# Performance work log

Measured on AMD Instinct MI355X. Metric: run time of the kernel, lower is better.

## Reference

```python
import jax, jax.numpy as jnp
import numpy as np


def conv1d(x, w, b, pad):
    # x: [B,C,T], w: [O,I,K]
    y = jax.lax.conv_general_dilated(x, w, (1,), [(pad, pad)],
                                     dimension_numbers=('NCH', 'OIH', 'NCH'))
    return y + b[None, :, None]


def setup_inputs() -> dict:
    key = jax.random.key(0)
    ks = jax.random.split(key, 16)
    s = 0.05
    return {
        'x':    jax.random.normal(ks[0], (1024, 512), dtype=jnp.float32),
        'w1':   jax.random.normal(ks[1], (5, 1, 3), dtype=jnp.float32) * s,
        'b1':   jnp.zeros((5,), jnp.float32),
        'w2':   jax.random.normal(ks[2], (10, 5, 5), dtype=jnp.float32) * s,
        'b2':   jnp.zeros((10,), jnp.float32),
        'w3':   jax.random.normal(ks[3], (10, 10, 7), dtype=jnp.float32) * s,
        'b3':   jnp.zeros((10,), jnp.float32),
        'code': jax.random.uniform(ks[4], (10, 32), dtype=jnp.float32),
        'd1w':  jax.random.normal(ks[5], (10, 10, 5), dtype=jnp.float32) * s,
        'd1b':  jnp.zeros((10,), jnp.float32),
        'd2w':  jax.random.normal(ks[6], (10, 10, 5), dtype=jnp.float32) * s,
        'd2b':  jnp.zeros((10,), jnp.float32),
        'fcw':  jax.random.normal(ks[7], (512, 5120), dtype=jnp.float32) * 0.01,
        'fcb':  jnp.zeros((512,), jnp.float32),
    }


def reference(x, w1, b1, w2, b2, w3, b3, code, d1w, d1b, d2w, d2b, fcw, fcb):
    B = x.shape[0]
    h = x[:, None, :]                                   # [B,1,512]
    h = jax.nn.relu(conv1d(h, w1, b1, 1))               # [B,5,512]
    h = jax.nn.relu(conv1d(h, w2, b2, 2))               # [B,10,512]
    h = jnp.tanh(conv1d(h, w3, b3, 3))                  # [B,10,512]
    # squared distance: sum_c (h[b,c,t] - code[c,k])^2 -> [B,512,32]
    x2 = jnp.sum(h * h, axis=1)                         # [B,512]
    cross = jnp.einsum('bct,ck->btk', h, code)          # [B,512,32]
    c2 = jnp.sum(code * code, axis=0)                   # [32]
    dist = x2[:, :, None] - 2.0 * cross + c2[None, None, :]
    prob = jax.nn.softmax(-dist, axis=-1)               # [B,512,32]
    q = jnp.einsum('btk,ck->btc', prob, code)           # [B,512,10]
    h = q.transpose(0, 2, 1)                            # [B,10,512]
    h = jax.nn.relu(conv1d(h, d1w, d1b, 2))
    h = jax.nn.relu(conv1d(h, d2w, d2b, 2))
    flat = h.reshape(B, -1)                             # [B,5120]
    return jnp.tanh(flat @ fcw.T + fcb)                 # [B,512]
```

## Files before the change

### kernel.cpp

```cpp
#include <hip/hip_runtime.h>
#include <hip/hip_bf16.h>

#define TT 512
#define XS 520
#define XH 4
#define RS 16
#define RH 8
#define NROW 528
#define K_FC 5120

typedef _Float16 hh2 __attribute__((ext_vector_type(2)));
typedef _Float16 h8 __attribute__((ext_vector_type(8)));
typedef float f32x16 __attribute__((ext_vector_type(16)));
typedef __attribute__((address_space(1))) const void GAS;
typedef __attribute__((address_space(3))) void LAS;

__device__ __forceinline__ float fast_tanh(float v) {
    float e = __expf(2.0f * v);
    return 1.0f - 2.0f / (e + 1.0f);
}
__device__ __forceinline__ unsigned pk(float a, float b) {
    return __builtin_bit_cast(unsigned, __builtin_amdgcn_cvt_pkrtz(a, b));
}

__global__ __launch_bounds__(256) void prep_kernel(
    const float* __restrict__ fcw, _Float16* __restrict__ fcw_h,
    const float* __restrict__ w2, const float* __restrict__ w3,
    const float* __restrict__ d1w, const float* __restrict__ d2w,
    const float* __restrict__ code, uint4* __restrict__ wtab,
    unsigned* __restrict__ c2tab)
{
    if (blockIdx.x < 1280) {
        int i = blockIdx.x * 256 + threadIdx.x;
        float4 a = ((const float4*)fcw)[i * 2];
        float4 b = ((const float4*)fcw)[i * 2 + 1];
        h8 v;
        v[0] = (_Float16)a.x; v[1] = (_Float16)a.y; v[2] = (_Float16)a.z; v[3] = (_Float16)a.w;
        v[4] = (_Float16)b.x; v[5] = (_Float16)b.y; v[6] = (_Float16)b.z; v[7] = (_Float16)b.w;
        *(h8*)&fcw_h[(size_t)i * 8] = v;
        return;
    }
    const int i = (blockIdx.x - 1280) * 256 + threadIdx.x;
    if (i < 1600) {
        const int lane = i & 63;
        const int o = lane & 31;
        const int hi = lane >> 5;
        h8 v = {};
        if (i < 320) {
            const int j = i >> 6;
            #pragma unroll
            for (int e = 0; e < 8; ++e) {
                int k = hi * 8 + e;
                if (o < 10 && k < 5) v[e] = (_Float16)w2[(o * 5 + k) * 5 + j];
            }
        } else if (i < 768) {
            const int j = (i - 320) >> 6;
            #pragma unroll
            for (int e = 0; e < 8; ++e) {
                int k = hi * 8 + e;
                if (o < 10 && k < 10) v[e] = (_Float16)w3[(o * 10 + k) * 7 + j];
            }
        } else if (i < 1088) {
            const int j = (i - 768) >> 6;
            #pragma unroll
            for (int e = 0; e < 8; ++e) {
                int k = hi * 8 + e;
                if (o < 10 && k < 10) v[e] = (_Float16)d1w[(o * 10 + k) * 5 + j];
            }
        } else if (i < 1408) {
            const int j = (i - 1088) >> 6;
            #pragma unroll
            for (int e = 0; e < 8; ++e) {
                int k = hi * 8 + e;
                if (o < 10 && k < 10) v[e] = (_Float16)d2w[(o * 10 + k) * 5 + j];
            }
        } else if (i < 1472) {
            #pragma unroll
            for (int e = 0; e < 8; ++e) {
                int ch = hi * 8 + e;
                if (ch < 10) v[e] = (_Float16)(2.0f * code[ch * 32 + o]);
            }
        } else {
            const int ks = (i - 1472) >> 6;
            #pragma unroll
            for (int e = 0; e < 8; ++e) {
                int kc = ks * 16 + hi * 8 + e;
                if (o < 10) v[e] = (_Float16)code[o * 32 + kc];
            }
        }
        wtab[i] = __builtin_bit_cast(uint4, v);
    } else if (i < 1632) {
        int k = i - 1600;
        float s = 0.f;
        for (int c = 0; c < 10; ++c) { float cv = code[c * 32 + k]; s = fmaf(cv, cv, s); }
        c2tab[k] = __float_as_uint(4.0f - s);
    }
}

template<int J, int P, int ACT>
__device__ __forceinline__ void conv_stage(
    const _Float16* __restrict__ src, _Float16* __restrict__ dst,
    const uint4* __restrict__ wtab, int wbase, const float* __restrict__ sb)
{
    const int tid = threadIdx.x;
    const int lane = tid & 63;
    const int wv = tid >> 6;
    const int l31 = lane & 31;
    const int hi = lane >> 5;

    uint4 wf[J];
    #pragma unroll
    for (int j = 0; j < J; ++j) wf[j] = wtab[wbase + j * 64 + lane];
    float bias[6];
    #pragma unroll
    for (int r = 0; r < 6; ++r) bias[r] = sb[(r & 3) + 8 * (r >> 2) + 4 * hi];

    #pragma unroll
    for (int tile = 0; tile < 4; ++tile) {
        const int tcol = wv * 128 + tile * 32 + l31;
        f32x16 acc = {};
        #pragma unroll
        for (int j = 0; j < J; ++j) {
            h8 bf = *(const h8*)(src + (tcol + RH - P + j) * RS + hi * 8);
            acc = __builtin_amdgcn_mfma_f32_32x32x16_f16(
                __builtin_bit_cast(h8, wf[j]), bf, acc, 0, 0, 0);
        }
        float v[6];
        #pragma unroll
        for (int r = 0; r < 6; ++r) {
            float t = acc[r] + bias[r];
            v[r] = (ACT == 0) ? fmaxf(t, 0.f) : fast_tanh(t);
        }
        unsigned* drow = (unsigned*)(dst + (tcol + RH) * RS);
        drow[hi * 2 + 0] = pk(v[0], v[1]);
        drow[hi * 2 + 1] = pk(v[2], v[3]);
        if (!hi) drow[4] = pk(v[4], v[5]);
    }
}

template<int J, int P>
__device__ __forceinline__ void conv_stage_flat(
    const _Float16* __restrict__ src, _Float16* __restrict__ flatrow,
    const uint4* __restrict__ wtab, int wbase, const float* __restrict__ sb)
{
    const int tid = threadIdx.x;
    const int lane = tid & 63;
    const int wv = tid >> 6;
    const int l31 = lane & 31;
    const int hi = lane >> 5;

    uint4 wf[J];
    #pragma unroll
    for (int j = 0; j < J; ++j) wf[j] = wtab[wbase + j * 64 + lane];
    float bias[6];
    #pragma unroll
    for (int r = 0; r < 6; ++r) bias[r] = sb[(r & 3) + 8 * (r >> 2) + 4 * hi];

    #pragma unroll
    for (int tile = 0; tile < 4; ++tile) {
        const int tcol = wv * 128 + tile * 32 + l31;
        f32x16 acc = {};
        #pragma unroll
        for (int j = 0; j < J; ++j) {
            h8 bf = *(const h8*)(src + (tcol + RH - P + j) * RS + hi * 8);
            acc = __builtin_amdgcn_mfma_f32_32x32x16_f16(
                __builtin_bit_cast(h8, wf[j]), bf, acc, 0, 0, 0);
        }
        #pragma unroll
        for (int r = 0; r < 4; ++r)
            flatrow[(r + 4 * hi) * TT + tcol] = (_Float16)fmaxf(acc[r] + bias[r], 0.f);
        if (!hi) {
            flatrow[8 * TT + tcol] = (_Float16)fmaxf(acc[4] + bias[4], 0.f);
            flatrow[9 * TT + tcol] = (_Float16)fmaxf(acc[5] + bias[5], 0.f);
        }
    }
}

__device__ __forceinline__ void vq_stage(
    const _Float16* __restrict__ src, _Float16* __restrict__ dst,
    const uint4* __restrict__ wtab, const float* __restrict__ sc2)
{
    const int tid = threadIdx.x;
    const int lane = tid & 63;
    const int wv = tid >> 6;
    const int l31 = lane & 31;
    const int hi = lane >> 5;

    const h8 wcr = __builtin_bit_cast(h8, wtab[1408 + lane]);
    const h8 wq0 = __builtin_bit_cast(h8, wtab[1472 + lane]);
    const h8 wq1 = __builtin_bit_cast(h8, wtab[1536 + lane]);
    float c2s[16];
    #pragma unroll
    for (int r = 0; r < 16; ++r) c2s[r] = sc2[(r & 3) + 8 * (r >> 2) + 4 * hi];

    #pragma unroll
    for (int tile = 0; tile < 4; ++tile) {
        const int tcol = wv * 128 + tile * 32 + l31;
        h8 bf = *(const h8*)(src + (tcol + RH) * RS + hi * 8);
        f32x16 sacc = {};
        sacc = __builtin_amdgcn_mfma_f32_32x32x16_f16(wcr, bf, sacc, 0, 0, 0);

        float e[16], sum = 0.f;
        #pragma unroll
        for (int r = 0; r < 16; ++r) { e[r] = __expf(sacc[r] + c2s[r]); sum += e[r]; }
        float denom = sum + __shfl_xor(sum, 32);
        float inv = 1.0f / denom;
        float so[16];
        #pragma unroll
        for (int r = 0; r < 16; ++r) so[r] = __shfl_xor(e[r], 32);

        float s0[8], s1[8];
        #pragma unroll
        for (int q = 0; q < 4; ++q) {
            s0[q]     = hi ? so[4 + q]  : e[q];
            s0[4 + q] = hi ? e[4 + q]   : so[q];
            s1[q]     = hi ? so[12 + q] : e[8 + q];
            s1[4 + q] = hi ? e[12 + q]  : so[8 + q];
        }
        uint4 b0u, b1u;
        b0u.x = pk(s0[0], s0[1]); b0u.y = pk(s0[2], s0[3]);
        b0u.z = pk(s0[4], s0[5]); b0u.w = pk(s0[6], s0[7]);
        b1u.x = pk(s1[0], s1[1]); b1u.y = pk(s1[2], s1[3]);
        b1u.z = pk(s1[4], s1[5]); b1u.w = pk(s1[6], s1[7]);

        f32x16 qacc = {};
        qacc = __builtin_amdgcn_mfma_f32_32x32x16_f16(wq0, __builtin_bit_cast(h8, b0u), qacc, 0, 0, 0);
        qacc = __builtin_amdgcn_mfma_f32_32x32x16_f16(wq1, __builtin_bit_cast(h8, b1u), qacc, 0, 0, 0);

        float v[6];
        #pragma unroll
        for (int r = 0; r < 6; ++r) v[r] = qacc[r] * inv;
        unsigned* drow = (unsigned*)(dst + (tcol + RH) * RS);
        drow[hi * 2 + 0] = pk(v[0], v[1]);
        drow[hi * 2 + 1] = pk(v[2], v[3]);
        if (!hi) drow[4] = pk(v[4], v[5]);
    }
}

__global__ __launch_bounds__(256, 4) void enc_dec_kernel(
    const float* __restrict__ x,
    const float* __restrict__ w1, const float* __restrict__ b1,
    const float* __restrict__ b2, const float* __restrict__ b3,
    const float* __restrict__ d1b, const float* __restrict__ d2b,
    const uint4* __restrict__ wtab, const unsigned* __restrict__ c2tab,
    _Float16* __restrict__ flat)
{
    __shared__ float xbuf[XS];
    __shared__ _Float16 bufA[NROW * RS];
    __shared__ _Float16 bufB[NROW * RS];
    __shared__ float sc2[32];
    __shared__ float sbias[4][16];

    const int tid = threadIdx.x;
    const int b = blockIdx.x;

    {
        uint4 z; z.x = 0; z.y = 0; z.z = 0; z.w = 0;
        uint4* pa = (uint4*)bufA;
        uint4* pb = (uint4*)bufB;
        for (int i = tid; i < NROW * RS / 8; i += 256) { pa[i] = z; pb[i] = z; }
    }
    if (tid < 8) xbuf[(tid < 4) ? tid : TT + tid] = 0.f;
    if (tid < 128)
        *(float4*)&xbuf[XH + tid * 4] = ((const float4*)(x + (size_t)b * TT))[tid];
    if (tid >= 128 && tid < 160) sc2[tid - 128] = __uint_as_float(c2tab[tid - 128]);
    if (tid >= 160 && tid < 224) {
        int s = (tid - 160) >> 4, i = (tid - 160) & 15;
        float v = 0.f;
        if (i < 10) v = (s == 0) ? b2[i] : (s == 1) ? b3[i] : (s == 2) ? d1b[i] : d2b[i];
        sbias[s][i] = v;
    }
    __syncthreads();

    {
        const int t0 = tid * 2;
        float xm = xbuf[XH + t0 - 1], x0v = xbuf[XH + t0];
        float x1v = xbuf[XH + t0 + 1], x2v = xbuf[XH + t0 + 2];
        h8 r0 = {}; h8 r1 = {};
        #pragma unroll
        for (int o = 0; o < 5; ++o) {
            float k0 = w1[o * 3], k1 = w1[o * 3 + 1], k2 = w1[o * 3 + 2], bb = b1[o];
            float a0 = fmaf(k0, xm,  fmaf(k1, x0v, fmaf(k2, x1v, bb)));
            float a1 = fmaf(k0, x0v, fmaf(k1, x1v, fmaf(k2, x2v, bb)));
            r0[o] = (_Float16)fmaxf(a0, 0.f);
            r1[o] = (_Float16)fmaxf(a1, 0.f);
        }
        *(h8*)&bufA[(t0 + RH) * RS] = r0;
        *(h8*)&bufA[(t0 + 1 + RH) * RS] = r1;
    }
    __syncthreads();

    conv_stage<5, 2, 0>(bufA, bufB, wtab, 0,    sbias[0]);
    __syncthreads();
    conv_stage<7, 3, 1>(bufB, bufA, wtab, 320,  sbias[1]);
    __syncthreads();
    vq_stage(bufA, bufB, wtab, sc2);
    __syncthreads();
    conv_stage<5, 2, 0>(bufB, bufA, wtab, 768,  sbias[2]);
    __syncthreads();
    conv_stage_flat<5, 2>(bufA, flat + (size_t)b * (10 * TT),
                          wtab, 1088, sbias[3]);
}

__global__ __launch_bounds__(256, 1) void fc_mfma_kernel(
    const _Float16* __restrict__ A,
    const _Float16* __restrict__ W,
    const float* __restrict__ bias,
    float* __restrict__ out)
{
    __shared__ __align__(16) unsigned char smem[49152];

    const int tid  = threadIdx.x;
    const int lane = tid & 63;
    const int w    = tid >> 6;

    const int bid = blockIdx.x;
    const int swz = (bid & 7) * 32 + (bid >> 3);
    const int m0 = (swz >> 4) * 64;
    const int n0 = (swz & 15) * 32;

    const int l31 = lane & 31;
    const int lh  = lane >> 5;
    const int rl16 = lane >> 4;
    const int c_lds = lane & 15;

    f32x16 acc0 = {}, acc1 = {};

    const _Float16* Asrc = A + (size_t)m0 * K_FC;
    const _Float16* Wsrc = W + (size_t)n0 * K_FC;

    auto stage = [&](int buf, int s) {
        unsigned char* Ad = smem + buf * 24576;
        unsigned char* Bd = Ad + 16384;
        const int k0 = s * 128;
        #pragma unroll
        for (int j = 0; j < 4; ++j) {
            const int i = w * 4 + j;
            const int rloc = 4 * i + rl16;
            const int csrc = c_lds ^ (rloc & 7);
            __builtin_amdgcn_global_load_lds(
                (GAS*)(Asrc + (size_t)rloc * K_FC + k0 + csrc * 8),
                (LAS*)(Ad + i * 1024), 16, 0, 0);
        }
        #pragma unroll
        for (int j = 0; j < 2; ++j) {
            const int i = w * 2 + j;
            const int rloc = 4 * i + rl16;
            const int csrc = c_lds ^ (rloc & 7);
            __builtin_amdgcn_global_load_lds(
                (GAS*)(Wsrc + (size_t)rloc * K_FC + k0 + csrc * 8),
                (LAS*)(Bd + i * 1024), 16, 0, 0);
        }
    };

    stage(0, 0);
    __syncthreads();

    for (int s = 0; s < 40; ++s) {
        const int cur = s & 1;
        if (s + 1 < 40) stage(cur ^ 1, s + 1);

        const unsigned char* Ab = smem + cur * 24576;
        const unsigned char* Bb = Ab + 16384;
        #pragma unroll
        for (int ks = 0; ks < 2; ++ks) {
            const int chunk = w * 4 + ks * 2 + lh;
            const int swzo  = ((chunk ^ (lane & 7)) << 4);
            h8 af0 = *(const h8*)(Ab +        l31 * 256 + swzo);
            h8 af1 = *(const h8*)(Ab + 8192 + l31 * 256 + swzo);
            h8 bf  = *(const h8*)(Bb +        l31 * 256 + swzo);
            acc0 = __builtin_amdgcn_mfma_f32_32x32x16_f16(af0, bf, acc0, 0, 0, 0);
            acc1 = __builtin_amdgcn_mfma_f32_32x32x16_f16(af1, bf, acc1, 0, 0, 0);
        }
        __syncthreads();
    }

    float* red = (float*)smem;
    {
        float* base = red + w * 2048;
        #pragma unroll
        for (int rq = 0; rq < 4; ++rq) {
            float4 v;
            v.x = acc0[rq*4+0]; v.y = acc0[rq*4+1]; v.z = acc0[rq*4+2]; v.w = acc0[rq*4+3];
            *(float4*)&base[rq * 256 + lane * 4] = v;
            v.x = acc1[rq*4+0]; v.y = acc1[rq*4+1]; v.z = acc1[rq*4+2]; v.w = acc1[rq*4+3];
            *(float4*)&base[1024 + rq * 256 + lane * 4] = v;
        }
    }
    __syncthreads();
    {
        const int lo   = tid & 63;
        const int mf   = (tid >> 6) & 1;
        const int half = tid >> 7;
        const int n    = lo & 31;
        const float bv = bias[n0 + n];
        #pragma unroll
        for (int q = 0; q < 2; ++q) {
            const int rq = half * 2 + q;
            const int idx = mf * 1024 + rq * 256 + lo * 4;
            float4 s0 = *(const float4*)&red[idx];
            float4 s1 = *(const float4*)&red[2048 + idx];
            float4 s2 = *(const float4*)&red[4096 + idx];
            float4 s3 = *(const float4*)&red[6144 + idx];
            #pragma unroll
            for (int rr = 0; rr < 4; ++rr) {
                float sum = ((const float*)&s0)[rr] + ((const float*)&s1)[rr]
                          + ((const float*)&s2)[rr] + ((const float*)&s3)[rr];
                const int m = mf * 32 + rr + 8 * rq + 4 * (lo >> 5);
                out[(size_t)(m0 + m) * 512 + n0 + n] = fast_tanh(sum + bv);
            }
        }
    }
}

extern "C" void kernel_launch(void* const* d_in, const int* in_sizes, int n_in,
                              void* d_out, int out_size, void* d_ws, size_t ws_size,
                              hipStream_t stream) {
    const float* x    = (const float*)d_in[0];
    const float* w1   = (const float*)d_in[1];
    const float* b1   = (const float*)d_in[2];
    const float* w2   = (const float*)d_in[3];
    const float* b2   = (const float*)d_in[4];
    const float* w3   = (const float*)d_in[5];
    const float* b3   = (const float*)d_in[6];
    const float* code = (const float*)d_in[7];
    const float* d1w  = (const float*)d_in[8];
    const float* d1b  = (const float*)d_in[9];
    const float* d2w  = (const float*)d_in[10];
    const float* d2b  = (const float*)d_in[11];
    const float* fcw  = (const float*)d_in[12];
    const float* fcb  = (const float*)d_in[13];
    float* out = (float*)d_out;

    _Float16* flat_h = (_Float16*)d_ws;
    _Float16* fcw_h  = (_Float16*)((char*)d_ws + 10485760);
    uint4*    wtab   = (uint4*)((char*)d_ws + 15728640);
    unsigned* c2tab  = (unsigned*)((char*)d_ws + 15728640 + 25600);

    const int Bsz = in_sizes[0] / TT;

    prep_kernel<<<1287, 256, 0, stream>>>(fcw, fcw_h, w2, w3, d1w, d2w, code,
                                          wtab, c2tab);
    enc_dec_kernel<<<Bsz, 256, 0, stream>>>(x, w1, b1, b2, b3, d1b, d2b,
                                            wtab, c2tab, flat_h);
    fc_mfma_kernel<<<256, 256, 0, stream>>>(flat_h, fcw_h, fcb, out);
}
```

Measured before the change: 55.02 us.

## Give each wave its own halo window to replace block barriers in encoder

Each wave now handles a 128-column slice of the sequence plus a 9-column halo in its own private LDS buffers. The block-wide __syncthreads between conv stages become wave barriers, at the cost of recomputing halo columns (5 MFMA tiles per stage instead of 4). Bias and codebook norms are read directly from global memory, dropping the shared staging. The fcw fp32-to-fp16 conversion is moved out of the prep kernel into extra blocks of the encoder kernel, so the prep launch becomes a small weight-table kernel.

Measured after the change: 57.91 us. 5.3% more time.

```diff
diff --git a/kernel.cpp b/kernel.cpp
--- a/kernel.cpp
+++ b/kernel.cpp
@@ -2,14 +2,9 @@
 #include <hip/hip_bf16.h>
 
 #define TT 512
-#define XS 520
-#define XH 4
-#define RS 16
-#define RH 8
-#define NROW 528
+#define RPW 152
 #define K_FC 5120
 
-typedef _Float16 hh2 __attribute__((ext_vector_type(2)));
 typedef _Float16 h8 __attribute__((ext_vector_type(8)));
 typedef float f32x16 __attribute__((ext_vector_type(16)));
 typedef __attribute__((address_space(1))) const void GAS;
@@ -22,25 +17,15 @@
 __device__ __forceinline__ unsigned pk(float a, float b) {
     return __builtin_bit_cast(unsigned, __builtin_amdgcn_cvt_pkrtz(a, b));
 }
-
-__global__ __launch_bounds__(256) void prep_kernel(
-    const float* __restrict__ fcw, _Float16* __restrict__ fcw_h,
+__device__ __forceinline__ void wfence() { __builtin_amdgcn_wave_barrier(); }
+
+__global__ __launch_bounds__(256) void prep_wtab_kernel(
     const float* __restrict__ w2, const float* __restrict__ w3,
     const float* __restrict__ d1w, const float* __restrict__ d2w,
     const float* __restrict__ code, uint4* __restrict__ wtab,
     unsigned* __restrict__ c2tab)
 {
-    if (blockIdx.x < 1280) {
-        int i = blockIdx.x * 256 + threadIdx.x;
-        float4 a = ((const float4*)fcw)[i * 2];
-        float4 b = ((const float4*)fcw)[i * 2 + 1];
-        h8 v;
-        v[0] = (_Float16)a.x; v[1] = (_Float16)a.y; v[2] = (_Float16)a.z; v[3] = (_Float16)a.w;
-        v[4] = (_Float16)b.x; v[5] = (_Float16)b.y; v[6] = (_Float16)b.z; v[7] = (_Float16)b.w;
-        *(h8*)&fcw_h[(size_t)i * 8] = v;
-        return;
-    }
-    const int i = (blockIdx.x - 1280) * 256 + threadIdx.x;
+    const int i = blockIdx.x * 256 + threadIdx.x;
     if (i < 1600) {
         const int lane = i & 63;
         const int o = lane & 31;
@@ -98,142 +83,155 @@
 }
 
 template<int J, int P, int ACT>
-__device__ __forceinline__ void conv_stage(
+__device__ __forceinline__ void conv_stage_p(
     const _Float16* __restrict__ src, _Float16* __restrict__ dst,
-    const uint4* __restrict__ wtab, int wbase, const float* __restrict__ sb)
-{
-    const int tid = threadIdx.x;
-    const int lane = tid & 63;
-    const int wv = tid >> 6;
+    const uint4* __restrict__ wtab, int wbase,
+    const float* __restrict__ bsrc, int vw0)
+{
+    const int lane = threadIdx.x & 63;
     const int l31 = lane & 31;
     const int hi = lane >> 5;
+    const int TS5[5] = {0, 32, 64, 96, 114};
 
     uint4 wf[J];
     #pragma unroll
     for (int j = 0; j < J; ++j) wf[j] = wtab[wbase + j * 64 + lane];
     float bias[6];
     #pragma unroll
-    for (int r = 0; r < 6; ++r) bias[r] = sb[(r & 3) + 8 * (r >> 2) + 4 * hi];
-
-    #pragma unroll
-    for (int tile = 0; tile < 4; ++tile) {
-        const int tcol = wv * 128 + tile * 32 + l31;
+    for (int r = 0; r < 6; ++r) {
+        int m = (r & 3) + 8 * (r >> 2) + 4 * hi;
+        bias[r] = (m < 10) ? bsrc[m] : 0.f;
+    }
+
+    #pragma unroll
+    for (int i = 0; i < 5; ++i) {
+        const int s = TS5[i];
+        const int row = s + 3 + l31;
         f32x16 acc = {};
         #pragma unroll
         for (int j = 0; j < J; ++j) {
-            h8 bf = *(const h8*)(src + (tcol + RH - P + j) * RS + hi * 8);
+            h8 bf = *(const h8*)(src + (row - P + j) * 16 + hi * 8);
             acc = __builtin_amdgcn_mfma_f32_32x32x16_f16(
                 __builtin_bit_cast(h8, wf[j]), bf, acc, 0, 0, 0);
         }
+        const int col = vw0 + s + l31;
+        const bool inb = (unsigned)col < 512u;
         float v[6];
         #pragma unroll
         for (int r = 0; r < 6; ++r) {
             float t = acc[r] + bias[r];
-            v[r] = (ACT == 0) ? fmaxf(t, 0.f) : fast_tanh(t);
-        }
-        unsigned* drow = (unsigned*)(dst + (tcol + RH) * RS);
-        drow[hi * 2 + 0] = pk(v[0], v[1]);
-        drow[hi * 2 + 1] = pk(v[2], v[3]);
-        if (!hi) drow[4] = pk(v[4], v[5]);
+            t = (ACT == 0) ? fmaxf(t, 0.f) : fast_tanh(t);
+            v[r] = inb ? t : 0.f;
+        }
+        uint2 s1v, s2v;
+        s1v.x = pk(v[0], v[1]); s1v.y = pk(v[2], v[3]);
+        s2v.x = hi ? 0u : pk(v[4], v[5]); s2v.y = 0u;
+        *(uint2*)(dst + row * 16 + 4 * hi) = s1v;
+        *(uint2*)(dst + row * 16 + 8 + 4 * hi) = s2v;
     }
 }
 
 template<int J, int P>
-__device__ __forceinline__ void conv_stage_flat(
+__device__ __forceinline__ void conv_stage_flat_p(
     const _Float16* __restrict__ src, _Float16* __restrict__ flatrow,
-    const uint4* __restrict__ wtab, int wbase, const float* __restrict__ sb)
-{
-    const int tid = threadIdx.x;
-    const int lane = tid & 63;
-    const int wv = tid >> 6;
+    const uint4* __restrict__ wtab, int wbase,
+    const float* __restrict__ bsrc, int vw0, int wcol0)
+{
+    const int lane = threadIdx.x & 63;
     const int l31 = lane & 31;
     const int hi = lane >> 5;
+    const int TS5[5] = {0, 32, 64, 96, 114};
 
     uint4 wf[J];
     #pragma unroll
     for (int j = 0; j < J; ++j) wf[j] = wtab[wbase + j * 64 + lane];
     float bias[6];
     #pragma unroll
-    for (int r = 0; r < 6; ++r) bias[r] = sb[(r & 3) + 8 * (r >> 2) + 4 * hi];
-
-    #pragma unroll
-    for (int tile = 0; tile < 4; ++tile) {
-        const int tcol = wv * 128 + tile * 32 + l31;
+    for (int r = 0; r < 6; ++r) {
+        int m = (r & 3) + 8 * (r >> 2) + 4 * hi;
+        bias[r] = (m < 10) ? bsrc[m] : 0.f;
+    }
+
+    #pragma unroll
+    for (int i = 0; i < 5; ++i) {
+        const int s = TS5[i];
+        const int row = s + 3 + l31;
         f32x16 acc = {};
         #pragma unroll
         for (int j = 0; j < J; ++j) {
-            h8 bf = *(const h8*)(src + (tcol + RH - P + j) * RS + hi * 8);
+            h8 bf = *(const h8*)(src + (row - P + j) * 16 + hi * 8);
             acc = __builtin_amdgcn_mfma_f32_32x32x16_f16(
                 __builtin_bit_cast(h8, wf[j]), bf, acc, 0, 0, 0);
         }
-        #pragma unroll
-        for (int r = 0; r < 4; ++r)
-            flatrow[(r + 4 * hi) * TT + tcol] = (_Float16)fmaxf(acc[r] + bias[r], 0.f);
-        if (!hi) {
-            flatrow[8 * TT + tcol] = (_Float16)fmaxf(acc[4] + bias[4], 0.f);
-            flatrow[9 * TT + tcol] = (_Float16)fmaxf(acc[5] + bias[5], 0.f);
-        }
-    }
-}
-
-__device__ __forceinline__ void vq_stage(
+        const int col = vw0 + s + l31;
+        if ((unsigned)(col - wcol0) < 128u) {
+            #pragma unroll
+            for (int r = 0; r < 4; ++r)
+                flatrow[(r + 4 * hi) * TT + col] = (_Float16)fmaxf(acc[r] + bias[r], 0.f);
+            if (!hi) {
+                flatrow[8 * TT + col] = (_Float16)fmaxf(acc[4] + bias[4], 0.f);
+                flatrow[9 * TT + col] = (_Float16)fmaxf(acc[5] + bias[5], 0.f);
+            }
+        }
+    }
+}
+
+__device__ __forceinline__ void vq_stage_p(
     const _Float16* __restrict__ src, _Float16* __restrict__ dst,
-    const uint4* __restrict__ wtab, const float* __restrict__ sc2)
-{
-    const int tid = threadIdx.x;
-    const int lane = tid & 63;
-    const int wv = tid >> 6;
+    const uint4* __restrict__ wtab, const unsigned* __restrict__ c2tab, int vw0)
+{
+    const int lane = threadIdx.x & 63;
     const int l31 = lane & 31;
     const int hi = lane >> 5;
+    const int TS5[5] = {0, 32, 64, 96, 114};
 
     const h8 wcr = __builtin_bit_cast(h8, wtab[1408 + lane]);
     const h8 wq0 = __builtin_bit_cast(h8, wtab[1472 + lane]);
     const h8 wq1 = __builtin_bit_cast(h8, wtab[1536 + lane]);
     float c2s[16];
     #pragma unroll
-    for (int r = 0; r < 16; ++r) c2s[r] = sc2[(r & 3) + 8 * (r >> 2) + 4 * hi];
-
-    #pragma unroll
-    for (int tile = 0; tile < 4; ++tile) {
-        const int tcol = wv * 128 + tile * 32 + l31;
-        h8 bf = *(const h8*)(src + (tcol + RH) * RS + hi * 8);
+    for (int r = 0; r < 16; ++r)
+        c2s[r] = __uint_as_float(c2tab[(r & 3) + 8 * (r >> 2) + 4 * hi]);
+
+    #pragma unroll
+    for (int i = 0; i < 5; ++i) {
+        const int s = TS5[i];
+        const int row = s + 3 + l31;
+        h8 bf = *(const h8*)(src + row * 16 + hi * 8);
         f32x16 sacc = {};
         sacc = __builtin_amdgcn_mfma_f32_32x32x16_f16(wcr, bf, sacc, 0, 0, 0);
 
         float e[16], sum = 0.f;
         #pragma unroll
         for (int r = 0; r < 16; ++r) { e[r] = __expf(sacc[r] + c2s[r]); sum += e[r]; }
-        float denom = sum + __shfl_xor(sum, 32);
-        float inv = 1.0f / denom;
-        float so[16];
-        #pragma unroll
-        for (int r = 0; r < 16; ++r) so[r] = __shfl_xor(e[r], 32);
-
-        float s0[8], s1[8];
-        #pragma unroll
-        for (int q = 0; q < 4; ++q) {
-            s0[q]     = hi ? so[4 + q]  : e[q];
-            s0[4 + q] = hi ? e[4 + q]   : so[q];
-            s1[q]     = hi ? so[12 + q] : e[8 + q];
-            s1[4 + q] = hi ? e[12 + q]  : so[8 + q];
-        }
+        float inv = 1.0f / (sum + __shfl_xor(sum, 32));
+
+        unsigned epk[8], sopk[8];
+        #pragma unroll
+        for (int q = 0; q < 8; ++q) epk[q] = pk(e[2 * q], e[2 * q + 1]);
+        #pragma unroll
+        for (int q = 0; q < 8; ++q) sopk[q] = (unsigned)__shfl_xor((int)epk[q], 32);
+
         uint4 b0u, b1u;
-        b0u.x = pk(s0[0], s0[1]); b0u.y = pk(s0[2], s0[3]);
-        b0u.z = pk(s0[4], s0[5]); b0u.w = pk(s0[6], s0[7]);
-        b1u.x = pk(s1[0], s1[1]); b1u.y = pk(s1[2], s1[3]);
-        b1u.z = pk(s1[4], s1[5]); b1u.w = pk(s1[6], s1[7]);
+        b0u.x = hi ? sopk[2] : epk[0]; b0u.y = hi ? sopk[3] : epk[1];
+        b0u.z = hi ? epk[2] : sopk[0]; b0u.w = hi ? epk[3] : sopk[1];
+        b1u.x = hi ? sopk[6] : epk[4]; b1u.y = hi ? sopk[7] : epk[5];
+        b1u.z = hi ? epk[6] : sopk[4]; b1u.w = hi ? epk[7] : sopk[5];
 
         f32x16 qacc = {};
         qacc = __builtin_amdgcn_mfma_f32_32x32x16_f16(wq0, __builtin_bit_cast(h8, b0u), qacc, 0, 0, 0);
         qacc = __builtin_amdgcn_mfma_f32_32x32x16_f16(wq1, __builtin_bit_cast(h8, b1u), qacc, 0, 0, 0);
 
+        const int col = vw0 + s + l31;
+        const bool inb = (unsigned)col < 512u;
         float v[6];
         #pragma unroll
-        for (int r = 0; r < 6; ++r) v[r] = qacc[r] * inv;
-        unsigned* drow = (unsigned*)(dst + (tcol + RH) * RS);
-        drow[hi * 2 + 0] = pk(v[0], v[1]);
-        drow[hi * 2 + 1] = pk(v[2], v[3]);
-        if (!hi) drow[4] = pk(v[4], v[5]);
+        for (int r = 0; r < 6; ++r) v[r] = inb ? qacc[r] * inv : 0.f;
+        uint2 s1v, s2v;
+        s1v.x = pk(v[0], v[1]); s1v.y = pk(v[2], v[3]);
+        s2v.x = hi ? 0u : pk(v[4], v[5]); s2v.y = 0u;
+        *(uint2*)(dst + row * 16 + 4 * hi) = s1v;
+        *(uint2*)(dst + row * 16 + 8 + 4 * hi) = s2v;
     }
 }
 
@@ -243,63 +241,77 @@
     const float* __restrict__ b2, const float* __restrict__ b3,
     const float* __restrict__ d1b, const float* __restrict__ d2b,
     const uint4* __restrict__ wtab, const unsigned* __restrict__ c2tab,
-    _Float16* __restrict__ flat)
-{
-    __shared__ float xbuf[XS];
-    __shared__ _Float16 bufA[NROW * RS];
-    __shared__ _Float16 bufB[NROW * RS];
-    __shared__ float sc2[32];
-    __shared__ float sbias[4][16];
+    _Float16* __restrict__ flat,
+    const float* __restrict__ fcw, _Float16* __restrict__ fcw_h, int nenc)
+{
+    __shared__ __align__(16) _Float16 wbuf[4][2][RPW * 16];
 
     const int tid = threadIdx.x;
-    const int b = blockIdx.x;
+    const int bid = blockIdx.x;
+
+    if (bid >= nenc) {
+        int i = (bid - nenc) * 256 + tid;
+        float4 a = ((const float4*)fcw)[i * 2];
+        float4 b4 = ((const float4*)fcw)[i * 2 + 1];
+        h8 v;
+        v[0] = (_Float16)a.x;  v[1] = (_Float16)a.y;
+        v[2] = (_Float16)a.z;  v[3] = (_Float16)a.w;
+        v[4] = (_Float16)b4.x; v[5] = (_Float16)b4.y;
+        v[6] = (_Float16)b4.z; v[7] = (_Float16)b4.w;
+        *(h8*)&fcw_h[(size_t)i * 8] = v;
+        return;
+    }
+
+    const int lane = tid & 63;
+    const int w = tid >> 6;
+    const int vw0 = w * 128 - 9;
+    _Float16* myA = wbuf[w][0];
+    _Float16* myB = wbuf[w][1];
+    const float* xrow = x + (size_t)bid * TT;
+
+    if (lane < 12) {
+        const int rz = (lane % 6 < 3) ? (lane % 6) : (146 + lane % 6);
+        _Float16* tb = (lane < 6) ? myA : myB;
+        uint4 z = {0, 0, 0, 0};
+        *(uint4*)(tb + rz * 16) = z;
+        *(uint4*)(tb + rz * 16 + 8) = z;
+    }
 
     {
-        uint4 z; z.x = 0; z.y = 0; z.z = 0; z.w = 0;
-        uint4* pa = (uint4*)bufA;
-        uint4* pb = (uint4*)bufB;
-        for (int i = tid; i < NROW * RS / 8; i += 256) { pa[i] = z; pb[i] = z; }
-    }
-    if (tid < 8) xbuf[(tid < 4) ? tid : TT + tid] = 0.f;
-    if (tid < 128)
-        *(float4*)&xbuf[XH + tid * 4] = ((const float4*)(x + (size_t)b * TT))[tid];
-    if (tid >= 128 && tid < 160) sc2[tid - 128] = __uint_as_float(c2tab[tid - 128]);
-    if (tid >= 160 && tid < 224) {
-        int s = (tid - 160) >> 4, i = (tid - 160) & 15;
-        float v = 0.f;
-        if (i < 10) v = (s == 0) ? b2[i] : (s == 1) ? b3[i] : (s == 2) ? d1b[i] : d2b[i];
-        sbias[s][i] = v;
-    }
-    __syncthreads();
-
-    {
-        const int t0 = tid * 2;
-        float xm = xbuf[XH + t0 - 1], x0v = xbuf[XH + t0];
-        float x1v = xbuf[XH + t0 + 1], x2v = xbuf[XH + t0 + 2];
-        h8 r0 = {}; h8 r1 = {};
-        #pragma unroll
-        for (int o = 0; o < 5; ++o) {
-            float k0 = w1[o * 3], k1 = w1[o * 3 + 1], k2 = w1[o * 3 + 2], bb = b1[o];
-            float a0 = fmaf(k0, xm,  fmaf(k1, x0v, fmaf(k2, x1v, bb)));
-            float a1 = fmaf(k0, x0v, fmaf(k1, x1v, fmaf(k2, x2v, bb)));
-            r0[o] = (_Float16)fmaxf(a0, 0.f);
-            r1[o] = (_Float16)fmaxf(a1, 0.f);
-        }
-        *(h8*)&bufA[(t0 + RH) * RS] = r0;
-        *(h8*)&bufA[(t0 + 1 + RH) * RS] = r1;
-    }
-    __syncthreads();
-
-    conv_stage<5, 2, 0>(bufA, bufB, wtab, 0,    sbias[0]);
-    __syncthreads();
-    conv_stage<7, 3, 1>(bufB, bufA, wtab, 320,  sbias[1]);
-    __syncthreads();
-    vq_stage(bufA, bufB, wtab, sc2);
-    __syncthreads();
-    conv_stage<5, 2, 0>(bufB, bufA, wtab, 768,  sbias[2]);
-    __syncthreads();
-    conv_stage_flat<5, 2>(bufA, flat + (size_t)b * (10 * TT),
-                          wtab, 1088, sbias[3]);
+        #pragma unroll
+        for (int it = 0; it < 3; ++it) {
+            const int off = lane + it * 64;
+            if (off < 146) {
+                const int col = vw0 + off;
+                float xm = ((unsigned)(col - 1) < 512u) ? xrow[col - 1] : 0.f;
+                float x0 = ((unsigned)col < 512u)       ? xrow[col]     : 0.f;
+                float xp = ((unsigned)(col + 1) < 512u) ? xrow[col + 1] : 0.f;
+                const bool inb = (unsigned)col < 512u;
+                h8 r0 = {};
+                #pragma unroll
+                for (int o = 0; o < 5; ++o) {
+                    float a = fmaf(w1[o * 3], xm,
+                              fmaf(w1[o * 3 + 1], x0,
+                              fmaf(w1[o * 3 + 2], xp, b1[o])));
+                    r0[o] = (_Float16)(inb ? fmaxf(a, 0.f) : 0.f);
+                }
+                *(h8*)(myA + (3 + off) * 16) = r0;
+                *(h8*)(myA + (3 + off) * 16 + 8) = (h8){};
+            }
+        }
+    }
+    wfence();
+
+    conv_stage_p<5, 2, 0>(myA, myB, wtab, 0,    b2,  vw0);
+    wfence();
+    conv_stage_p<7, 3, 1>(myB, myA, wtab, 320,  b3,  vw0);
+    wfence();
+    vq_stage_p(myA, myB, wtab, c2tab, vw0);
+    wfence();
+    conv_stage_p<5, 2, 0>(myB, myA, wtab, 768,  d1b, vw0);
+    wfence();
+    conv_stage_flat_p<5, 2>(myA, flat + (size_t)bid * (10 * TT),
+                            wtab, 1088, d2b, vw0, w * 128);
 }
 
 __global__ __launch_bounds__(256, 1) void fc_mfma_kernel(
@@ -439,9 +451,9 @@
 
     const int Bsz = in_sizes[0] / TT;
 
-    prep_kernel<<<1287, 256, 0, stream>>>(fcw, fcw_h, w2, w3, d1w, d2w, code,
-                                          wtab, c2tab);
-    enc_dec_kernel<<<Bsz, 256, 0, stream>>>(x, w1, b1, b2, b3, d1b, d2b,
-                                            wtab, c2tab, flat_h);
+    prep_wtab_kernel<<<7, 256, 0, stream>>>(w2, w3, d1w, d2w, code, wtab, c2tab);
+    enc_dec_kernel<<<Bsz + 1280, 256, 0, stream>>>(x, w1, b1, b2, b3, d1b, d2b,
+                                                   wtab, c2tab, flat_h,
+                                                   fcw, fcw_h, Bsz);
     fc_mfma_kernel<<<256, 256, 0, stream>>>(flat_h, fcw_h, fcb, out);
 }
```

## Overlap fc weight fp16 conversion with encoder blocks and trim shared-memory setup

Applied to the files above, without the earlier changes.

Moves the fcw float-to-half conversion out of the prep kernel and into extra blocks of the encoder/decoder kernel, so the conversion runs concurrently with the per-sample conv/VQ work. The prep kernel then only builds the small weight tables. The encoder also drops the x staging buffer and shared bias and c2 copies, reading them straight from global memory, zeroes only the halo rows of bufA, and packs softmax values to fp16 before the cross-lane shuffle, which halves the number of shuffles. The tile loops are unrolled by 2 instead of fully, which may lower register pressure but also reduces ILP.

Result: no change. 55.24 us (+0.4%).

```diff
diff --git a/kernel.cpp b/kernel.cpp
--- a/kernel.cpp
+++ b/kernel.cpp
@@ -2,14 +2,11 @@
 #include <hip/hip_bf16.h>
 
 #define TT 512
-#define XS 520
-#define XH 4
 #define RS 16
 #define RH 8
 #define NROW 528
 #define K_FC 5120
 
-typedef _Float16 hh2 __attribute__((ext_vector_type(2)));
 typedef _Float16 h8 __attribute__((ext_vector_type(8)));
 typedef float f32x16 __attribute__((ext_vector_type(16)));
 typedef __attribute__((address_space(1))) const void GAS;
@@ -23,24 +20,13 @@
     return __builtin_bit_cast(unsigned, __builtin_amdgcn_cvt_pkrtz(a, b));
 }
 
-__global__ __launch_bounds__(256) void prep_kernel(
-    const float* __restrict__ fcw, _Float16* __restrict__ fcw_h,
+__global__ __launch_bounds__(256) void prep_wtab_kernel(
     const float* __restrict__ w2, const float* __restrict__ w3,
     const float* __restrict__ d1w, const float* __restrict__ d2w,
     const float* __restrict__ code, uint4* __restrict__ wtab,
     unsigned* __restrict__ c2tab)
 {
-    if (blockIdx.x < 1280) {
-        int i = blockIdx.x * 256 + threadIdx.x;
-        float4 a = ((const float4*)fcw)[i * 2];
-        float4 b = ((const float4*)fcw)[i * 2 + 1];
-        h8 v;
-        v[0] = (_Float16)a.x; v[1] = (_Float16)a.y; v[2] = (_Float16)a.z; v[3] = (_Float16)a.w;
-        v[4] = (_Float16)b.x; v[5] = (_Float16)b.y; v[6] = (_Float16)b.z; v[7] = (_Float16)b.w;
-        *(h8*)&fcw_h[(size_t)i * 8] = v;
-        return;
-    }
-    const int i = (blockIdx.x - 1280) * 256 + threadIdx.x;
+    const int i = blockIdx.x * 256 + threadIdx.x;
     if (i < 1600) {
         const int lane = i & 63;
         const int o = lane & 31;
@@ -100,7 +86,7 @@
 template<int J, int P, int ACT>
 __device__ __forceinline__ void conv_stage(
     const _Float16* __restrict__ src, _Float16* __restrict__ dst,
-    const uint4* __restrict__ wtab, int wbase, const float* __restrict__ sb)
+    const uint4* __restrict__ wtab, int wbase, const float* __restrict__ bsrc)
 {
     const int tid = threadIdx.x;
     const int lane = tid & 63;
@@ -113,9 +99,12 @@
     for (int j = 0; j < J; ++j) wf[j] = wtab[wbase + j * 64 + lane];
     float bias[6];
     #pragma unroll
-    for (int r = 0; r < 6; ++r) bias[r] = sb[(r & 3) + 8 * (r >> 2) + 4 * hi];
-
-    #pragma unroll
+    for (int r = 0; r < 6; ++r) {
+        int m = (r & 3) + 8 * (r >> 2) + 4 * hi;
+        bias[r] = (m < 10) ? bsrc[m] : 0.f;
+    }
+
+    #pragma unroll 2
     for (int tile = 0; tile < 4; ++tile) {
         const int tcol = wv * 128 + tile * 32 + l31;
         f32x16 acc = {};
@@ -141,7 +130,7 @@
 template<int J, int P>
 __device__ __forceinline__ void conv_stage_flat(
     const _Float16* __restrict__ src, _Float16* __restrict__ flatrow,
-    const uint4* __restrict__ wtab, int wbase, const float* __restrict__ sb)
+    const uint4* __restrict__ wtab, int wbase, const float* __restrict__ bsrc)
 {
     const int tid = threadIdx.x;
     const int lane = tid & 63;
@@ -154,9 +143,12 @@
     for (int j = 0; j < J; ++j) wf[j] = wtab[wbase + j * 64 + lane];
     float bias[6];
     #pragma unroll
-    for (int r = 0; r < 6; ++r) bias[r] = sb[(r & 3) + 8 * (r >> 2) + 4 * hi];
-
-    #pragma unroll
+    for (int r = 0; r < 6; ++r) {
+        int m = (r & 3) + 8 * (r >> 2) + 4 * hi;
+        bias[r] = (m < 10) ? bsrc[m] : 0.f;
+    }
+
+    #pragma unroll 2
     for (int tile = 0; tile < 4; ++tile) {
         const int tcol = wv * 128 + tile * 32 + l31;
         f32x16 acc = {};
@@ -178,7 +170,7 @@
 
 __device__ __forceinline__ void vq_stage(
     const _Float16* __restrict__ src, _Float16* __restrict__ dst,
-    const uint4* __restrict__ wtab, const float* __restrict__ sc2)
+    const uint4* __restrict__ wtab, const unsigned* __restrict__ c2tab)
 {
     const int tid = threadIdx.x;
     const int lane = tid & 63;
@@ -191,9 +183,10 @@
     const h8 wq1 = __builtin_bit_cast(h8, wtab[1536 + lane]);
     float c2s[16];
     #pragma unroll
-    for (int r = 0; r < 16; ++r) c2s[r] = sc2[(r & 3) + 8 * (r >> 2) + 4 * hi];
-
-    #pragma unroll
+    for (int r = 0; r < 16; ++r)
+        c2s[r] = __uint_as_float(c2tab[(r & 3) + 8 * (r >> 2) + 4 * hi]);
+
+    #pragma unroll 2
     for (int tile = 0; tile < 4; ++tile) {
         const int tcol = wv * 128 + tile * 32 + l31;
         h8 bf = *(const h8*)(src + (tcol + RH) * RS + hi * 8);
@@ -203,25 +196,19 @@
         float e[16], sum = 0.f;
         #pragma unroll
         for (int r = 0; r < 16; ++r) { e[r] = __expf(sacc[r] + c2s[r]); sum += e[r]; }
-        float denom = sum + __shfl_xor(sum, 32);
-        float inv = 1.0f / denom;
-        float so[16];
-        #pragma unroll
-        for (int r = 0; r < 16; ++r) so[r] = __shfl_xor(e[r], 32);
-
-        float s0[8], s1[8];
-        #pragma unroll
-        for (int q = 0; q < 4; ++q) {
-            s0[q]     = hi ? so[4 + q]  : e[q];
-            s0[4 + q] = hi ? e[4 + q]   : so[q];
-            s1[q]     = hi ? so[12 + q] : e[8 + q];
-            s1[4 + q] = hi ? e[12 + q]  : so[8 + q];
-        }
+        float inv = 1.0f / (sum + __shfl_xor(sum, 32));
+
+        unsigned epk[8], sopk[8];
+        #pragma unroll
+        for (int q = 0; q < 8; ++q) epk[q] = pk(e[2 * q], e[2 * q + 1]);
+        #pragma unroll
+        for (int q = 0; q < 8; ++q) sopk[q] = (unsigned)__shfl_xor((int)epk[q], 32);
+
         uint4 b0u, b1u;
-        b0u.x = pk(s0[0], s0[1]); b0u.y = pk(s0[2], s0[3]);
-        b0u.z = pk(s0[4], s0[5]); b0u.w = pk(s0[6], s0[7]);
-        b1u.x = pk(s1[0], s1[1]); b1u.y = pk(s1[2], s1[3]);
-        b1u.z = pk(s1[4], s1[5]); b1u.w = pk(s1[6], s1[7]);
+        b0u.x = hi ? sopk[2] : epk[0]; b0u.y = hi ? sopk[3] : epk[1];
+        b0u.z = hi ? epk[2] : sopk[0]; b0u.w = hi ? epk[3] : sopk[1];
+        b1u.x = hi ? sopk[6] : epk[4]; b1u.y = hi ? sopk[7] : epk[5];
+        b1u.z = hi ? epk[6] : sopk[4]; b1u.w = hi ? epk[7] : sopk[5];
 
         f32x16 qacc = {};
         qacc = __builtin_amdgcn_mfma_f32_32x32x16_f16(wq0, __builtin_bit_cast(h8, b0u), qacc, 0, 0, 0);
@@ -243,63 +230,74 @@
     const float* __restrict__ b2, const float* __restrict__ b3,
     const float* __restrict__ d1b, const float* __restrict__ d2b,
     const uint4* __restrict__ wtab, const unsigned* __restrict__ c2tab,
-    _Float16* __restrict__ flat)
-{
-    __shared__ float xbuf[XS];
-    __shared__ _Float16 bufA[NROW * RS];
-    __shared__ _Float16 bufB[NROW * RS];
-    __shared__ float sc2[32];
-    __shared__ float sbias[4][16];
+    _Float16* __restrict__ flat,
+    const float* __restrict__ fcw, _Float16* __restrict__ fcw_h, int nenc)
+{
+    __shared__ __align__(16) _Float16 bufA[NROW * RS];
+    __shared__ __align__(16) _Float16 bufB[NROW * RS];
 
     const int tid = threadIdx.x;
-    const int b = blockIdx.x;
-
+    const int bid = blockIdx.x;
+
+    if (bid >= nenc) {
+        int i = (bid - nenc) * 256 + tid;
+        float4 a = ((const float4*)fcw)[i * 2];
+        float4 b4 = ((const float4*)fcw)[i * 2 + 1];
+        h8 v;
+        v[0] = (_Float16)a.x;  v[1] = (_Float16)a.y;
+        v[2] = (_Float16)a.z;  v[3] = (_Float16)a.w;
+        v[4] = (_Float16)b4.x; v[5] = (_Float16)b4.y;
+        v[6] = (_Float16)b4.z; v[7] = (_Float16)b4.w;
+        *(h8*)&fcw_h[(size_t)i * 8] = v;
+        return;
+    }
+
+    if (tid < 32) {
+        int r = tid >> 1, half = tid & 1;
+        int row = (r < 8) ? r : 512 + r;
+        uint4 z = {0, 0, 0, 0};
+        *(uint4*)(bufA + row * RS + half * 8) = z;
+    }
     {
-        uint4 z; z.x = 0; z.y = 0; z.z = 0; z.w = 0;
-        uint4* pa = (uint4*)bufA;
+        uint4 z = {0, 0, 0, 0};
         uint4* pb = (uint4*)bufB;
-        for (int i = tid; i < NROW * RS / 8; i += 256) { pa[i] = z; pb[i] = z; }
-    }
-    if (tid < 8) xbuf[(tid < 4) ? tid : TT + tid] = 0.f;
-    if (tid < 128)
-        *(float4*)&xbuf[XH + tid * 4] = ((const float4*)(x + (size_t)b * TT))[tid];
-    if (tid >= 128 && tid < 160) sc2[tid - 128] = __uint_as_float(c2tab[tid - 128]);
-    if (tid >= 160 && tid < 224) {
-        int s = (tid - 160) >> 4, i = (tid - 160) & 15;
-        float v = 0.f;
-        if (i < 10) v = (s == 0) ? b2[i] : (s == 1) ? b3[i] : (s == 2) ? d1b[i] : d2b[i];
-        sbias[s][i] = v;
-    }
-    __syncthreads();
+        for (int i = tid; i < NROW * RS / 8; i += 256) pb[i] = z;
+    }
 
     {
+        const float* xrow = x + (size_t)bid * TT;
         const int t0 = tid * 2;
-        float xm = xbuf[XH + t0 - 1], x0v = xbuf[XH + t0];
-        float x1v = xbuf[XH + t0 + 1], x2v = xbuf[XH + t0 + 2];
-        h8 r0 = {}; h8 r1 = {};
+        float xm  = (t0 > 0) ? xrow[t0 - 1] : 0.f;
+        float x0v = xrow[t0];
+        float x1v = xrow[t0 + 1];
+        float xp  = (t0 < TT - 2) ? xrow[t0 + 2] : 0.f;
+        h8 r0 = {}, r1 = {};
         #pragma unroll
         for (int o = 0; o < 5; ++o) {
             float k0 = w1[o * 3], k1 = w1[o * 3 + 1], k2 = w1[o * 3 + 2], bb = b1[o];
             float a0 = fmaf(k0, xm,  fmaf(k1, x0v, fmaf(k2, x1v, bb)));
-            float a1 = fmaf(k0, x0v, fmaf(k1, x1v, fmaf(k2, x2v, bb)));
+            float a1 = fmaf(k0, x0v, fmaf(k1, x1v, fmaf(k2, xp,  bb)));
             r0[o] = (_Float16)fmaxf(a0, 0.f);
             r1[o] = (_Float16)fmaxf(a1, 0.f);
         }
+        h8 zz = {};
         *(h8*)&bufA[(t0 + RH) * RS] = r0;
+        *(h8*)&bufA[(t0 + RH) * RS + 8] = zz;
         *(h8*)&bufA[(t0 + 1 + RH) * RS] = r1;
-    }
-    __syncthreads();
-
-    conv_stage<5, 2, 0>(bufA, bufB, wtab, 0,    sbias[0]);
-    __syncthreads();
-    conv_stage<7, 3, 1>(bufB, bufA, wtab, 320,  sbias[1]);
-    __syncthreads();
-    vq_stage(bufA, bufB, wtab, sc2);
-    __syncthreads();
-    conv_stage<5, 2, 0>(bufB, bufA, wtab, 768,  sbias[2]);
-    __syncthreads();
-    conv_stage_flat<5, 2>(bufA, flat + (size_t)b * (10 * TT),
-                          wtab, 1088, sbias[3]);
+        *(h8*)&bufA[(t0 + 1 + RH) * RS + 8] = zz;
+    }
+    __syncthreads();
+
+    conv_stage<5, 2, 0>(bufA, bufB, wtab, 0,    b2);
+    __syncthreads();
+    conv_stage<7, 3, 1>(bufB, bufA, wtab, 320,  b3);
+    __syncthreads();
+    vq_stage(bufA, bufB, wtab, c2tab);
+    __syncthreads();
+    conv_stage<5, 2, 0>(bufB, bufA, wtab, 768,  d1b);
+    __syncthreads();
+    conv_stage_flat<5, 2>(bufA, flat + (size_t)bid * (10 * TT),
+                          wtab, 1088, d2b);
 }
 
 __global__ __launch_bounds__(256, 1) void fc_mfma_kernel(
@@ -439,9 +437,9 @@
 
     const int Bsz = in_sizes[0] / TT;
 
-    prep_kernel<<<1287, 256, 0, stream>>>(fcw, fcw_h, w2, w3, d1w, d2w, code,
-                                          wtab, c2tab);
-    enc_dec_kernel<<<Bsz, 256, 0, stream>>>(x, w1, b1, b2, b3, d1b, d2b,
-                                            wtab, c2tab, flat_h);
+    prep_wtab_kernel<<<7, 256, 0, stream>>>(w2, w3, d1w, d2w, code, wtab, c2tab);
+    enc_dec_kernel<<<Bsz + 1280, 256, 0, stream>>>(x, w1, b1, b2, b3, d1b, d2b,
+                                                   wtab, c2tab, flat_h,
+                                                   fcw, fcw_h, Bsz);
     fc_mfma_kernel<<<256, 256, 0, stream>>>(flat_h, fcw_h, fcb, out);
 }
```
